# Performance work log

Hardware: AMD Instinct MI355X
Metric: run time of the kernel (lower is better)

## Reference

```python
import jax, jax.numpy as jnp
import numpy as np

B, N, E = 2, 50000, 800000
F_IN, H1, C1, C2 = 1433, 8, 8, 7
NEG_SLOPE = 0.2
EPS = 1e-16


def _gat_conv(x, edge_index, W, a_src, a_dst, b, heads, out_ch):
    # x: [N, F_in]; edge_index: [2, E] (row0 = source j, row1 = target i, PyG convention)
    n = x.shape[0]
    loops = jnp.arange(n)
    src = jnp.concatenate([edge_index[0], loops])  # add self-loops (PyG default)
    dst = jnp.concatenate([edge_index[1], loops])
    h = (x @ W).reshape(n, heads, out_ch)                       # [N, H, C]
    e_src = (h * a_src).sum(-1)                                 # [N, H]
    e_dst = (h * a_dst).sum(-1)                                 # [N, H]
    e = jax.nn.leaky_relu(e_src[src] + e_dst[dst], NEG_SLOPE)   # [E', H]
    # segment softmax over incoming edges of each destination node
    m = jax.ops.segment_max(e, dst, num_segments=n)             # [N, H]
    ex = jnp.exp(e - m[dst])
    den = jax.ops.segment_sum(ex, dst, num_segments=n)
    alpha = ex / (den[dst] + EPS)                               # [E', H]
    out = jax.ops.segment_sum(h[src] * alpha[:, :, None], dst, num_segments=n)  # [N, H, C]
    return out.reshape(n, heads * out_ch) + b


def setup_inputs() -> dict:
    key = jax.random.key(0)
    ks = jax.random.split(key, 8)
    x = jax.random.normal(ks[0], (B, N, F_IN), dtype=jnp.float32)
    edge_index = jax.random.randint(ks[1], (B, 2, E), 0, N, dtype=jnp.int64)
    s1 = 1.0 / np.sqrt(F_IN)
    s2 = 1.0 / np.sqrt(H1 * C1)
    return {
        "x": x,
        "edge_index": edge_index,
        "W1": jax.random.normal(ks[2], (F_IN, H1 * C1), dtype=jnp.float32) * s1,
        "a1_src": jax.random.normal(ks[3], (H1, C1), dtype=jnp.float32) * 0.3,
        "a1_dst": jax.random.normal(ks[4], (H1, C1), dtype=jnp.float32) * 0.3,
        "b1": jnp.zeros((H1 * C1,), dtype=jnp.float32),
        "W2": jax.random.normal(ks[5], (H1 * C1, C2), dtype=jnp.float32) * s2,
        "a2_src": jax.random.normal(ks[6], (1, C2), dtype=jnp.float32) * 0.3,
        "a2_dst": jax.random.normal(ks[7], (1, C2), dtype=jnp.float32) * 0.3,
        "b2": jnp.zeros((C2,), dtype=jnp.float32),
    }


def reference(x, edge_index, W1, a1_src, a1_dst, b1, W2, a2_src, a2_dst, b2):
    # Eval mode: dropout (p=0.6) is identity.
    def per_graph(xi, ei):
        h = _gat_conv(xi, ei, W1, a1_src, a1_dst, b1, H1, C1)   # [N, 64]
        h = jax.nn.elu(h)
        o = _gat_conv(h, ei, W2, a2_src, a2_dst, b2, 1, C2)     # [N, 7]
        return jax.nn.log_softmax(o, axis=-1)
    return jax.vmap(per_graph)(x, edge_index)
```

## Files before the change

kernel.cpp:

```cpp
#include <hip/hip_runtime.h>
#include <hip/hip_bf16.h>
#include <math.h>

#define NB 2
#define NN 50000
#define NE 800000
#define FIN 1433
#define KPAD 1440
#define HD 64
#define C2c 7
#define NCHUNK 196

typedef __attribute__((ext_vector_type(8))) short short8;
typedef __attribute__((ext_vector_type(4))) float f32x4;
typedef f32x4 __attribute__((aligned(4))) f32x4u;

static __device__ __forceinline__ float leaky(float e) { return e > 0.f ? e : 0.2f * e; }

static __device__ __forceinline__ short bf16r(float f) {
    __hip_bfloat16 h = __float2bfloat16(f);
    return *reinterpret_cast<short*>(&h);
}
static __device__ __forceinline__ float bf2f(short s) {
    unsigned u = ((unsigned)(unsigned short)s) << 16;
    return __uint_as_float(u);
}

__global__ __launch_bounds__(256) void w1t_kernel(const float* __restrict__ W,
                                                  short* __restrict__ Bt) {
    int i = blockIdx.x * 256 + threadIdx.x;
    if (i >= 64 * KPAD) return;
    int c = i / KPAD, k = i - c * KPAD;
    float v = (k < FIN) ? W[k * 64 + c] : 0.f;
    Bt[i] = bf16r(v);
}

__global__ __launch_bounds__(256) void gemm1_mfma(const float* __restrict__ x,
                                                  const short* __restrict__ Bt,
                                                  short* __restrict__ h1b) {
    const int b = blockIdx.y;
    const int wave = threadIdx.x >> 6;
    const int lane = threadIdx.x & 63;
    const int m = lane & 15;
    const int quad = lane >> 4;
    const int row0 = blockIdx.x * 128 + wave * 32;

    const float* xb = x + (size_t)b * NN * FIN;
    short* hb = h1b + (size_t)b * NN * HD;

    int r0 = row0 + m;
    int r1 = row0 + 16 + m;
    int r0c = r0 < NN ? r0 : NN - 1;
    int r1c = r1 < NN ? r1 : NN - 1;
    const float* a0p = xb + (size_t)r0c * FIN + quad * 8;
    const float* a1p = xb + (size_t)r1c * FIN + quad * 8;
    const short* btp = Bt + quad * 8 + (size_t)m * KPAD;

    f32x4 acc[2][4];
#pragma unroll
    for (int t = 0; t < 2; t++)
#pragma unroll
        for (int n = 0; n < 4; n++) acc[t][n] = (f32x4){0.f, 0.f, 0.f, 0.f};

    for (int kt = 0; kt < 1408; kt += 32) {
        f32x4 af00 = *(const f32x4u*)(a0p + kt);
        f32x4 af01 = *(const f32x4u*)(a0p + kt + 4);
        f32x4 af10 = *(const f32x4u*)(a1p + kt);
        f32x4 af11 = *(const f32x4u*)(a1p + kt + 4);
        short8 fa0, fa1;
        fa0[0] = bf16r(af00[0]); fa0[1] = bf16r(af00[1]); fa0[2] = bf16r(af00[2]); fa0[3] = bf16r(af00[3]);
        fa0[4] = bf16r(af01[0]); fa0[5] = bf16r(af01[1]); fa0[6] = bf16r(af01[2]); fa0[7] = bf16r(af01[3]);
        fa1[0] = bf16r(af10[0]); fa1[1] = bf16r(af10[1]); fa1[2] = bf16r(af10[2]); fa1[3] = bf16r(af10[3]);
        fa1[4] = bf16r(af11[0]); fa1[5] = bf16r(af11[1]); fa1[6] = bf16r(af11[2]); fa1[7] = bf16r(af11[3]);
#pragma unroll
        for (int n = 0; n < 4; n++) {
            short8 fb = *(const short8*)(btp + (size_t)n * 16 * KPAD + kt);
            acc[0][n] = __builtin_amdgcn_mfma_f32_16x16x32_bf16(fa0, fb, acc[0][n], 0, 0, 0);
            acc[1][n] = __builtin_amdgcn_mfma_f32_16x16x32_bf16(fa1, fb, acc[1][n], 0, 0, 0);
        }
    }
    {
        short8 fa0, fa1;
#pragma unroll
        for (int j = 0; j < 8; j++) {
            int k = 1408 + quad * 8 + j;
            fa0[j] = bf16r(k < FIN ? a0p[1408 + j] : 0.f);
            fa1[j] = bf16r(k < FIN ? a1p[1408 + j] : 0.f);
        }
#pragma unroll
        for (int n = 0; n < 4; n++) {
            short8 fb = *(const short8*)(btp + (size_t)n * 16 * KPAD + 1408);
            acc[0][n] = __builtin_amdgcn_mfma_f32_16x16x32_bf16(fa0, fb, acc[0][n], 0, 0, 0);
            acc[1][n] = __builtin_amdgcn_mfma_f32_16x16x32_bf16(fa1, fb, acc[1][n], 0, 0, 0);
        }
    }
#pragma unroll
    for (int t = 0; t < 2; t++) {
#pragma unroll
        for (int r = 0; r < 4; r++) {
            int row = row0 + t * 16 + quad * 4 + r;
            if (row < NN) {
#pragma unroll
                for (int n = 0; n < 4; n++) hb[(size_t)row * HD + n * 16 + m] = bf16r(acc[t][n][r]);
            }
        }
    }
}

__global__ void coef1_kernel(const short* __restrict__ h1b, const float* __restrict__ a_src,
                             const float* __restrict__ a_dst, float* __restrict__ es,
                             float* __restrict__ ed) {
    int i = blockIdx.x * blockDim.x + threadIdx.x;
    if (i >= NB * NN * 8) return;
    int h = i & 7;
    int n = i >> 3;
    const short8 hv = *(const short8*)(h1b + (size_t)n * 64 + h * 8);
    float s = 0.f, d = 0.f;
#pragma unroll
    for (int c = 0; c < 8; c++) {
        float v = bf2f(hv[c]);
        s += v * a_src[h * 8 + c];
        d += v * a_dst[h * 8 + c];
    }
    es[i] = s;
    ed[i] = d;
}

__global__ void deg_kernel(const int* __restrict__ ei, int* __restrict__ deg) {
    int i = blockIdx.x * blockDim.x + threadIdx.x;
    if (i >= NB * NE) return;
    int b = i / NE, e = i - b * NE;
    int dst = ei[(size_t)b * 2 * NE + NE + e];
    atomicAdd(deg + b * NN + dst, 1);
}

__global__ __launch_bounds__(256) void scan1_kernel(const int* __restrict__ deg,
                                                    int* __restrict__ rowptr,
                                                    int* __restrict__ bsum) {
    const int b = blockIdx.y, th = threadIdx.x;
    const int i = blockIdx.x * 256 + th;
    __shared__ int s[256];
    int v = (i < NN) ? deg[b * NN + i] : 0;
    s[th] = v;
    __syncthreads();
    int val = v;
    for (int off = 1; off < 256; off <<= 1) {
        int t = (th >= off) ? s[th - off] : 0;
        __syncthreads();
        val += t;
        s[th] = val;
        __syncthreads();
    }
    if (i < NN) rowptr[b * (NN + 1) + i] = val - v;
    if (th == 255) bsum[b * NCHUNK + blockIdx.x] = val;
}

__global__ __launch_bounds__(256) void scan2_kernel(const int* __restrict__ bsum,
                                                    int* __restrict__ boff,
                                                    int* __restrict__ rowptr) {
    const int b = blockIdx.x, th = threadIdx.x;
    __shared__ int s[256];
    int v = (th < NCHUNK) ? bsum[b * NCHUNK + th] : 0;
    s[th] = v;
    __syncthreads();
    int val = v;
    for (int off = 1; off < 256; off <<= 1) {
        int t = (th >= off) ? s[th - off] : 0;
        __syncthreads();
        val += t;
        s[th] = val;
        __syncthreads();
    }
    if (th < NCHUNK) boff[b * NCHUNK + th] = val - v;
    if (th == 255) rowptr[b * (NN + 1) + NN] = val;
}

__global__ __launch_bounds__(256) void scan3_kernel(const int* __restrict__ boff,
                                                    int* __restrict__ rowptr,
                                                    int* __restrict__ cursor) {
    const int b = blockIdx.y;
    const int i = blockIdx.x * 256 + threadIdx.x;
    if (i >= NN) return;
    int r = rowptr[b * (NN + 1) + i] + boff[b * NCHUNK + blockIdx.x];
    rowptr[b * (NN + 1) + i] = r;
    cursor[b * NN + i] = r;
}

__global__ void scatter_kernel(const int* __restrict__ ei, int* __restrict__ cursor,
                               int* __restrict__ col) {
    int i = blockIdx.x * blockDim.x + threadIdx.x;
    if (i >= NB * NE) return;
    int b = i / NE, e = i - b * NE;
    int src = ei[(size_t)b * 2 * NE + e];
    int dst = ei[(size_t)b * 2 * NE + NE + e];
    int pos = atomicAdd(cursor + b * NN + dst, 1);
    col[(size_t)b * NE + pos] = src;
}

__global__ __launch_bounds__(256) void agg1_kernel(
    const short* __restrict__ h1b, const float* __restrict__ es, const float* __restrict__ ed,
    const float* __restrict__ b1, const float* __restrict__ W2, const float* __restrict__ a2s,
    const float* __restrict__ a2d, const int* __restrict__ rowptr, const int* __restrict__ col,
    float* __restrict__ h2, float* __restrict__ es2, float* __restrict__ ed2) {
    int w = blockIdx.x * 4 + (threadIdx.x >> 6);
    if (w >= NB * NN) return;
    const int lane = threadIdx.x & 63;
    const int s = lane >> 3;
    const int cg = lane & 7;
    const int b = w / NN;
    const int n = w - b * NN;
    const size_t nb = (size_t)b * NN;

    const float edv = ed[(nb + n) * 8 + cg];
    float den = 0.f;
    float acc[8];
#pragma unroll
    for (int j = 0; j < 8; j++) acc[j] = 0.f;

    if (s == 0) {
        float e = leaky(es[(nb + n) * 8 + cg] + edv);
        float wv = __expf(e);
        den = wv;
        const short8 hv = *(const short8*)(h1b + (nb + n) * 64 + cg * 8);
#pragma unroll
        for (int j = 0; j < 8; j++) acc[j] = wv * bf2f(hv[j]);
    }

    const int* cp = col + (size_t)b * NE;
    const int start = rowptr[b * (NN + 1) + n];
    const int end = rowptr[b * (NN + 1) + n + 1];
    for (int idx = start + s; idx < end; idx += 8) {
        int src = cp[idx];
        float e = leaky(es[(nb + src) * 8 + cg] + edv);
        float wv = __expf(e);
        den += wv;
        const short8 hv = *(const short8*)(h1b + (nb + src) * 64 + cg * 8);
#pragma unroll
        for (int j = 0; j < 8; j++) acc[j] += wv * bf2f(hv[j]);
    }

#pragma unroll
    for (int off = 8; off < 64; off <<= 1) {
        den += __shfl_xor(den, off, 64);
#pragma unroll
        for (int j = 0; j < 8; j++) acc[j] += __shfl_xor(acc[j], off, 64);
    }

    const float inv = 1.f / (den + 1e-16f);
    float g[8];
#pragma unroll
    for (int j = 0; j < 8; j++) {
        float o = acc[j] * inv + b1[cg * 8 + j];
        g[j] = o > 0.f ? o : expm1f(o);
    }

    float p[7];
#pragma unroll
    for (int c2 = 0; c2 < 7; c2++) {
        float v = 0.f;
#pragma unroll
        for (int j = 0; j < 8; j++) v += g[j] * W2[(cg * 8 + j) * 7 + c2];
        p[c2] = v;
    }
#pragma unroll
    for (int off = 1; off < 8; off <<= 1) {
#pragma unroll
        for (int c2 = 0; c2 < 7; c2++) p[c2] += __shfl_xor(p[c2], off, 64);
    }
    if (lane == 0) {
        float4 v0 = make_float4(p[0], p[1], p[2], p[3]);
        float4 v1 = make_float4(p[4], p[5], p[6], 0.f);
        *(float4*)&h2[(nb + n) * 8] = v0;
        *(float4*)&h2[(nb + n) * 8 + 4] = v1;
        float s2 = 0.f, d2 = 0.f;
#pragma unroll
        for (int c2 = 0; c2 < 7; c2++) {
            s2 += p[c2] * a2s[c2];
            d2 += p[c2] * a2d[c2];
        }
        es2[nb + n] = s2;
        ed2[nb + n] = d2;
    }
}

__global__ void agg2_kernel(const float* __restrict__ h2, const float* __restrict__ es2,
                            const float* __restrict__ ed2, const float* __restrict__ b2,
                            const int* __restrict__ rowptr, const int* __restrict__ col,
                            float* __restrict__ out) {
    int i = blockIdx.x * blockDim.x + threadIdx.x;
    if (i >= NB * NN) return;
    const int b = i / NN;
    const int n = i - b * NN;
    const size_t nb = (size_t)b * NN;
    const float edv = ed2[nb + n];
    float acc0 = 0, acc1 = 0, acc2 = 0, acc3 = 0, acc4 = 0, acc5 = 0, acc6 = 0, den = 0;
    {
        float e = leaky(es2[nb + n] + edv);
        float wv = __expf(e);
        den += wv;
        const float4 u0 = *(const float4*)&h2[(nb + n) * 8];
        const float4 u1 = *(const float4*)&h2[(nb + n) * 8 + 4];
        acc0 += wv * u0.x; acc1 += wv * u0.y; acc2 += wv * u0.z; acc3 += wv * u0.w;
        acc4 += wv * u1.x; acc5 += wv * u1.y; acc6 += wv * u1.z;
    }
    const int* cp = col + (size_t)b * NE;
    const int start = rowptr[b * (NN + 1) + n];
    const int end = rowptr[b * (NN + 1) + n + 1];
    for (int idx = start; idx < end; idx++) {
        int src = cp[idx];
        float e = leaky(es2[nb + src] + edv);
        float wv = __expf(e);
        den += wv;
        const float4 u0 = *(const float4*)&h2[(nb + src) * 8];
        const float4 u1 = *(const float4*)&h2[(nb + src) * 8 + 4];
        acc0 += wv * u0.x; acc1 += wv * u0.y; acc2 += wv * u0.z; acc3 += wv * u0.w;
        acc4 += wv * u1.x; acc5 += wv * u1.y; acc6 += wv * u1.z;
    }
    float inv = 1.f / (den + 1e-16f);
    float o[7];
    o[0] = acc0 * inv + b2[0]; o[1] = acc1 * inv + b2[1]; o[2] = acc2 * inv + b2[2];
    o[3] = acc3 * inv + b2[3]; o[4] = acc4 * inv + b2[4]; o[5] = acc5 * inv + b2[5];
    o[6] = acc6 * inv + b2[6];
    float m = o[0];
#pragma unroll
    for (int c = 1; c < 7; c++) m = fmaxf(m, o[c]);
    float sum = 0.f;
#pragma unroll
    for (int c = 0; c < 7; c++) sum += expf(o[c] - m);
    float lse = m + logf(sum);
    float* op = out + ((size_t)b * NN + n) * 7;
#pragma unroll
    for (int c = 0; c < 7; c++) op[c] = o[c] - lse;
}

extern "C" void kernel_launch(void* const* d_in, const int* in_sizes, int n_in,
                              void* d_out, int out_size, void* d_ws, size_t ws_size,
                              hipStream_t stream) {
    const float* x = (const float*)d_in[0];
    const int* ei = (const int*)d_in[1];
    const float* W1 = (const float*)d_in[2];
    const float* a1s = (const float*)d_in[3];
    const float* a1d = (const float*)d_in[4];
    const float* b1 = (const float*)d_in[5];
    const float* W2 = (const float*)d_in[6];
    const float* a2s = (const float*)d_in[7];
    const float* a2d = (const float*)d_in[8];
    const float* b2 = (const float*)d_in[9];
    float* out = (float*)d_out;

    char* ws = (char*)d_ws;
    size_t off = 0;
    auto alloc = [&](size_t bytes) {
        void* p = ws + off;
        off += (bytes + 255) & ~(size_t)255;
        return p;
    };
    short* h1b = (short*)alloc((size_t)NB * NN * 64 * 2);
    float* es1 = (float*)alloc((size_t)NB * NN * 8 * 4);
    float* ed1 = (float*)alloc((size_t)NB * NN * 8 * 4);
    float* h2 = (float*)alloc((size_t)NB * NN * 8 * 4);
    float* es2 = (float*)alloc((size_t)NB * NN * 4);
    float* ed2 = (float*)alloc((size_t)NB * NN * 4);
    int* rowptr = (int*)alloc((size_t)NB * (NN + 1) * 4);
    int* cursor = (int*)alloc((size_t)NB * NN * 4);
    int* deg = (int*)alloc((size_t)NB * NN * 4);
    int* col = (int*)alloc((size_t)NB * NE * 4);
    short* Bt = (short*)alloc((size_t)64 * KPAD * 2);
    int* bsum = (int*)alloc((size_t)NB * NCHUNK * 4);
    int* boff = (int*)alloc((size_t)NB * NCHUNK * 4);

    hipMemsetAsync(deg, 0, (size_t)NB * NN * 4, stream);

    w1t_kernel<<<(64 * KPAD + 255) / 256, 256, 0, stream>>>(W1, Bt);

    dim3 ggrid((NN + 127) / 128, NB);
    gemm1_mfma<<<ggrid, 256, 0, stream>>>(x, Bt, h1b);

    coef1_kernel<<<(NB * NN * 8 + 255) / 256, 256, 0, stream>>>(h1b, a1s, a1d, es1, ed1);

    deg_kernel<<<(NB * NE + 255) / 256, 256, 0, stream>>>(ei, deg);
    dim3 sgrid(NCHUNK, NB);
    scan1_kernel<<<sgrid, 256, 0, stream>>>(deg, rowptr, bsum);
    scan2_kernel<<<NB, 256, 0, stream>>>(bsum, boff, rowptr);
    scan3_kernel<<<sgrid, 256, 0, stream>>>(boff, rowptr, cursor);
    scatter_kernel<<<(NB * NE + 255) / 256, 256, 0, stream>>>(ei, cursor, col);

    agg1_kernel<<<(NB * NN + 3) / 4, 256, 0, stream>>>(h1b, es1, ed1, b1, W2, a2s, a2d,
                                                       rowptr, col, h2, es2, ed2);
    agg2_kernel<<<(NB * NN + 255) / 256, 256, 0, stream>>>(h2, es2, ed2, b2, rowptr, col, out);
}
```

Baseline: 1.211 ms.

## Fuse attention coefficient computation into aggregation and parallelize layer-2 gather

Removes the separate coef1 kernel and the es/ed buffers. Attention logits for both layers are now recomputed inside the aggregation kernels from the gathered features, so the per-edge es gather goes away. The cost is a few extra dot products per edge. agg2 now uses 8 lanes per node with a shuffle reduction instead of one thread per node, which adds parallelism and latency hiding for the edge gather.

```diff
diff --git a/kernel.cpp b/kernel.cpp
--- a/kernel.cpp
+++ b/kernel.cpp
@@ -105,25 +105,6 @@
             }
         }
     }
-}
-
-__global__ void coef1_kernel(const short* __restrict__ h1b, const float* __restrict__ a_src,
-                             const float* __restrict__ a_dst, float* __restrict__ es,
-                             float* __restrict__ ed) {
-    int i = blockIdx.x * blockDim.x + threadIdx.x;
-    if (i >= NB * NN * 8) return;
-    int h = i & 7;
-    int n = i >> 3;
-    const short8 hv = *(const short8*)(h1b + (size_t)n * 64 + h * 8);
-    float s = 0.f, d = 0.f;
-#pragma unroll
-    for (int c = 0; c < 8; c++) {
-        float v = bf2f(hv[c]);
-        s += v * a_src[h * 8 + c];
-        d += v * a_dst[h * 8 + c];
-    }
-    es[i] = s;
-    ed[i] = d;
 }
 
 __global__ void deg_kernel(const int* __restrict__ ei, int* __restrict__ deg) {
@@ -198,10 +179,10 @@
 }
 
 __global__ __launch_bounds__(256) void agg1_kernel(
-    const short* __restrict__ h1b, const float* __restrict__ es, const float* __restrict__ ed,
-    const float* __restrict__ b1, const float* __restrict__ W2, const float* __restrict__ a2s,
-    const float* __restrict__ a2d, const int* __restrict__ rowptr, const int* __restrict__ col,
-    float* __restrict__ h2, float* __restrict__ es2, float* __restrict__ ed2) {
+    const short* __restrict__ h1b, const float* __restrict__ a1s, const float* __restrict__ a1d,
+    const float* __restrict__ b1, const float* __restrict__ W2,
+    const int* __restrict__ rowptr, const int* __restrict__ col,
+    float* __restrict__ h2) {
     int w = blockIdx.x * 4 + (threadIdx.x >> 6);
     if (w >= NB * NN) return;
     const int lane = threadIdx.x & 63;
@@ -211,19 +192,29 @@
     const int n = w - b * NN;
     const size_t nb = (size_t)b * NN;
 
-    const float edv = ed[(nb + n) * 8 + cg];
+    float as[8], ad[8];
+#pragma unroll
+    for (int j = 0; j < 8; j++) { as[j] = a1s[cg * 8 + j]; ad[j] = a1d[cg * 8 + j]; }
+
+    const short8 hself = *(const short8*)(h1b + (nb + n) * 64 + cg * 8);
+    float edv = 0.f, e_self = 0.f;
+#pragma unroll
+    for (int j = 0; j < 8; j++) {
+        float v = bf2f(hself[j]);
+        edv += v * ad[j];
+        e_self += v * as[j];
+    }
+
     float den = 0.f;
     float acc[8];
 #pragma unroll
     for (int j = 0; j < 8; j++) acc[j] = 0.f;
 
     if (s == 0) {
-        float e = leaky(es[(nb + n) * 8 + cg] + edv);
-        float wv = __expf(e);
+        float wv = __expf(leaky(e_self + edv));
         den = wv;
-        const short8 hv = *(const short8*)(h1b + (nb + n) * 64 + cg * 8);
-#pragma unroll
-        for (int j = 0; j < 8; j++) acc[j] = wv * bf2f(hv[j]);
+#pragma unroll
+        for (int j = 0; j < 8; j++) acc[j] = wv * bf2f(hself[j]);
     }
 
     const int* cp = col + (size_t)b * NE;
@@ -231,12 +222,15 @@
     const int end = rowptr[b * (NN + 1) + n + 1];
     for (int idx = start + s; idx < end; idx += 8) {
         int src = cp[idx];
-        float e = leaky(es[(nb + src) * 8 + cg] + edv);
-        float wv = __expf(e);
+        const short8 hv = *(const short8*)(h1b + (nb + src) * 64 + cg * 8);
+        float fv[8];
+        float e = 0.f;
+#pragma unroll
+        for (int j = 0; j < 8; j++) { fv[j] = bf2f(hv[j]); e += fv[j] * as[j]; }
+        float wv = __expf(leaky(e + edv));
         den += wv;
-        const short8 hv = *(const short8*)(h1b + (nb + src) * 64 + cg * 8);
-#pragma unroll
-        for (int j = 0; j < 8; j++) acc[j] += wv * bf2f(hv[j]);
+#pragma unroll
+        for (int j = 0; j < 8; j++) acc[j] += wv * fv[j];
     }
 
 #pragma unroll
@@ -272,65 +266,86 @@
         float4 v1 = make_float4(p[4], p[5], p[6], 0.f);
         *(float4*)&h2[(nb + n) * 8] = v0;
         *(float4*)&h2[(nb + n) * 8 + 4] = v1;
-        float s2 = 0.f, d2 = 0.f;
-#pragma unroll
-        for (int c2 = 0; c2 < 7; c2++) {
-            s2 += p[c2] * a2s[c2];
-            d2 += p[c2] * a2d[c2];
-        }
-        es2[nb + n] = s2;
-        ed2[nb + n] = d2;
-    }
-}
-
-__global__ void agg2_kernel(const float* __restrict__ h2, const float* __restrict__ es2,
-                            const float* __restrict__ ed2, const float* __restrict__ b2,
-                            const int* __restrict__ rowptr, const int* __restrict__ col,
-                            float* __restrict__ out) {
-    int i = blockIdx.x * blockDim.x + threadIdx.x;
-    if (i >= NB * NN) return;
-    const int b = i / NN;
-    const int n = i - b * NN;
+    }
+}
+
+__global__ __launch_bounds__(256) void agg2_kernel(
+    const float* __restrict__ h2, const float* __restrict__ a2s, const float* __restrict__ a2d,
+    const float* __restrict__ b2, const int* __restrict__ rowptr, const int* __restrict__ col,
+    float* __restrict__ out) {
+    int g = blockIdx.x * 32 + (threadIdx.x >> 3);
+    if (g >= NB * NN) return;
+    const int l = threadIdx.x & 7;
+    const int b = g / NN;
+    const int n = g - b * NN;
     const size_t nb = (size_t)b * NN;
-    const float edv = ed2[nb + n];
-    float acc0 = 0, acc1 = 0, acc2 = 0, acc3 = 0, acc4 = 0, acc5 = 0, acc6 = 0, den = 0;
-    {
-        float e = leaky(es2[nb + n] + edv);
-        float wv = __expf(e);
-        den += wv;
-        const float4 u0 = *(const float4*)&h2[(nb + n) * 8];
-        const float4 u1 = *(const float4*)&h2[(nb + n) * 8 + 4];
-        acc0 += wv * u0.x; acc1 += wv * u0.y; acc2 += wv * u0.z; acc3 += wv * u0.w;
-        acc4 += wv * u1.x; acc5 += wv * u1.y; acc6 += wv * u1.z;
-    }
+
+    float sc[7], dc[7];
+#pragma unroll
+    for (int c = 0; c < 7; c++) { sc[c] = a2s[c]; dc[c] = a2d[c]; }
+
+    const float4 su0 = *(const float4*)&h2[(nb + n) * 8];
+    const float4 su1 = *(const float4*)&h2[(nb + n) * 8 + 4];
+    float self7[7] = {su0.x, su0.y, su0.z, su0.w, su1.x, su1.y, su1.z};
+    float edv = 0.f;
+#pragma unroll
+    for (int c = 0; c < 7; c++) edv += self7[c] * dc[c];
+
+    float acc[7];
+#pragma unroll
+    for (int c = 0; c < 7; c++) acc[c] = 0.f;
+    float den = 0.f;
+
+    if (l == 0) {
+        float es = 0.f;
+#pragma unroll
+        for (int c = 0; c < 7; c++) es += self7[c] * sc[c];
+        float wv = __expf(leaky(es + edv));
+        den = wv;
+#pragma unroll
+        for (int c = 0; c < 7; c++) acc[c] = wv * self7[c];
+    }
+
     const int* cp = col + (size_t)b * NE;
     const int start = rowptr[b * (NN + 1) + n];
     const int end = rowptr[b * (NN + 1) + n + 1];
-    for (int idx = start; idx < end; idx++) {
+    for (int idx = start + l; idx < end; idx += 8) {
         int src = cp[idx];
-        float e = leaky(es2[nb + src] + edv);
-        float wv = __expf(e);
-        den += wv;
         const float4 u0 = *(const float4*)&h2[(nb + src) * 8];
         const float4 u1 = *(const float4*)&h2[(nb + src) * 8 + 4];
-        acc0 += wv * u0.x; acc1 += wv * u0.y; acc2 += wv * u0.z; acc3 += wv * u0.w;
-        acc4 += wv * u1.x; acc5 += wv * u1.y; acc6 += wv * u1.z;
-    }
-    float inv = 1.f / (den + 1e-16f);
-    float o[7];
-    o[0] = acc0 * inv + b2[0]; o[1] = acc1 * inv + b2[1]; o[2] = acc2 * inv + b2[2];
-    o[3] = acc3 * inv + b2[3]; o[4] = acc4 * inv + b2[4]; o[5] = acc5 * inv + b2[5];
-    o[6] = acc6 * inv + b2[6];
-    float m = o[0];
-#pragma unroll
-    for (int c = 1; c < 7; c++) m = fmaxf(m, o[c]);
-    float sum = 0.f;
-#pragma unroll
-    for (int c = 0; c < 7; c++) sum += expf(o[c] - m);
-    float lse = m + logf(sum);
-    float* op = out + ((size_t)b * NN + n) * 7;
-#pragma unroll
-    for (int c = 0; c < 7; c++) op[c] = o[c] - lse;
+        float v7[7] = {u0.x, u0.y, u0.z, u0.w, u1.x, u1.y, u1.z};
+        float es = 0.f;
+#pragma unroll
+        for (int c = 0; c < 7; c++) es += v7[c] * sc[c];
+        float wv = __expf(leaky(es + edv));
+        den += wv;
+#pragma unroll
+        for (int c = 0; c < 7; c++) acc[c] += wv * v7[c];
+    }
+
+#pragma unroll
+    for (int off = 1; off < 8; off <<= 1) {
+        den += __shfl_xor(den, off, 64);
+#pragma unroll
+        for (int c = 0; c < 7; c++) acc[c] += __shfl_xor(acc[c], off, 64);
+    }
+
+    if (l == 0) {
+        const float inv = 1.f / (den + 1e-16f);
+        float o[7];
+#pragma unroll
+        for (int c = 0; c < 7; c++) o[c] = acc[c] * inv + b2[c];
+        float m = o[0];
+#pragma unroll
+        for (int c = 1; c < 7; c++) m = fmaxf(m, o[c]);
+        float sum = 0.f;
+#pragma unroll
+        for (int c = 0; c < 7; c++) sum += expf(o[c] - m);
+        float lse = m + logf(sum);
+        float* op = out + ((size_t)b * NN + n) * 7;
+#pragma unroll
+        for (int c = 0; c < 7; c++) op[c] = o[c] - lse;
+    }
 }
 
 extern "C" void kernel_launch(void* const* d_in, const int* in_sizes, int n_in,
@@ -356,11 +371,7 @@
         return p;
     };
     short* h1b = (short*)alloc((size_t)NB * NN * 64 * 2);
-    float* es1 = (float*)alloc((size_t)NB * NN * 8 * 4);
-    float* ed1 = (float*)alloc((size_t)NB * NN * 8 * 4);
     float* h2 = (float*)alloc((size_t)NB * NN * 8 * 4);
-    float* es2 = (float*)alloc((size_t)NB * NN * 4);
-    float* ed2 = (float*)alloc((size_t)NB * NN * 4);
     int* rowptr = (int*)alloc((size_t)NB * (NN + 1) * 4);
     int* cursor = (int*)alloc((size_t)NB * NN * 4);
     int* deg = (int*)alloc((size_t)NB * NN * 4);
@@ -376,8 +387,6 @@
     dim3 ggrid((NN + 127) / 128, NB);
     gemm1_mfma<<<ggrid, 256, 0, stream>>>(x, Bt, h1b);
 
-    coef1_kernel<<<(NB * NN * 8 + 255) / 256, 256, 0, stream>>>(h1b, a1s, a1d, es1, ed1);
-
     deg_kernel<<<(NB * NE + 255) / 256, 256, 0, stream>>>(ei, deg);
     dim3 sgrid(NCHUNK, NB);
     scan1_kernel<<<sgrid, 256, 0, stream>>>(deg, rowptr, bsum);
@@ -385,7 +394,8 @@
     scan3_kernel<<<sgrid, 256, 0, stream>>>(boff, rowptr, cursor);
     scatter_kernel<<<(NB * NE + 255) / 256, 256, 0, stream>>>(ei, cursor, col);
 
-    agg1_kernel<<<(NB * NN + 3) / 4, 256, 0, stream>>>(h1b, es1, ed1, b1, W2, a2s, a2d,
-                                                       rowptr, col, h2, es2, ed2);
-    agg2_kernel<<<(NB * NN + 255) / 256, 256, 0, stream>>>(h2, es2, ed2, b2, rowptr, col, out);
-}
+    agg1_kernel<<<(NB * NN + 3) / 4, 256, 0, stream>>>(h1b, a1s, a1d, b1, W2,
+                                                       rowptr, col, h2);
+    agg2_kernel<<<(NB * NN * 8 + 255) / 256, 256, 0, stream>>>(h2, a2s, a2d, b2,
+                                                               rowptr, col, out);
+}
```

Result: faster. 1.183 ms (-2.3%).
